# Kernel optimization log

Hardware: AMD Instinct MI355X
Metric: run time of the kernel (lower is better)

## Reference

```python
import jax, jax.numpy as jnp
import numpy as np

B, T, D, U = 8, 1024, 128, 2048
LEAK = 0.5       # leak_rate
EXPONENT = 2     # PowerIndex exponent
POW_INDEX = 2    # square neurons whose index % POW_INDEX == 0


def setup_inputs() -> dict:
    key = jax.random.key(0)
    k1, k2, k3, k4 = jax.random.split(key, 4)
    inputs = jax.random.normal(k1, (B, T, D), dtype=jnp.float32)
    # input-to-reservoir weights (InputMatrix ~ scaled dense here)
    w_in = jax.random.normal(k2, (D, U), dtype=jnp.float32) * (1.0 / np.sqrt(D))
    b_in = jax.random.uniform(k3, (U,), dtype=jnp.float32, minval=-0.05, maxval=0.05)
    # reservoir kernel (ErdosRenyi sparse random; dense surrogate scaled to
    # spectral radius ~0.9 via 0.9/sqrt(U))
    w_res = jax.random.normal(k4, (U, U), dtype=jnp.float32) * (0.9 / np.sqrt(U))
    return {"inputs": inputs, "w_in": w_in, "b_in": b_in, "w_res": w_res}


def reference(inputs, w_in, b_in, w_res):
    # Leaky ESN recurrence scanned over time:
    a = jnp.asarray(LEAK, inputs.dtype)
    # Precompute the input projection for all timesteps in one big GEMM.
    proj = jnp.einsum('btd,du->btu', inputs, w_in) + b_in  # [B,T,U]

    def step(state, p_t):  # state: [B,U], p_t: [B,U]
        pre = p_t + state @ w_res
        new = (1.0 - a) * state + a * jnp.tanh(pre)
        return new, new

    s0 = jnp.zeros((inputs.shape[0], w_res.shape[0]), inputs.dtype)
    _, states = jax.lax.scan(step, s0, jnp.swapaxes(proj, 0, 1))  # [T,B,U]
    states = jnp.swapaxes(states, 0, 1)  # [B,T,U]

    # PowerIndex: raise neurons at every POW_INDEX-th position to EXPONENT
    idx = jnp.arange(states.shape[-1])
    powered = jnp.where(idx % POW_INDEX == 0, states ** EXPONENT, states)

    # raw=False: concat input with reservoir output along features
    return jnp.concatenate([inputs, powered], axis=-1)  # [B,T,D+U]
```

## Files before the change

### kernel.cpp

```cpp
#include <hip/hip_runtime.h>
#include <cmath>

typedef __attribute__((ext_vector_type(8))) short short8;
typedef __attribute__((ext_vector_type(4))) float f32x4;
typedef __attribute__((ext_vector_type(2))) unsigned short us2;
typedef unsigned long long u64;
typedef unsigned int u32;

__device__ __forceinline__ unsigned short f2bf(float x){
  u32 u = __float_as_uint(x);
  u32 r = u + 0x7FFFu + ((u >> 16) & 1u);
  return (unsigned short)(r >> 16);
}

__global__ void bswz_kernel(const float* __restrict__ wres,
                            const float* __restrict__ win,
                            unsigned short* __restrict__ B){
  int tid = blockIdx.x * 256 + threadIdx.x;
  int l   = tid & 63;
  int cf  = tid >> 6;
  int f   = cf % 34;
  int gk  = cf / 34;
  int ks  = gk & 1;
  int gcg = gk >> 1;
  int col = (gcg << 4) + (l & 15);
  int k0  = ks * 1088 + (f << 5) + ((l >> 4) << 3);
  short8 vv;
  #pragma unroll
  for (int j = 0; j < 8; ++j){
    int k = k0 + j;
    float v = (k < 2048) ? wres[(size_t)k * 2048 + col]
                         : win[(size_t)(k - 2048) * 2048 + col];
    vv[j] = (short)f2bf(v);
  }
  *((short8*)(B + (size_t)tid * 8)) = vv;
}

__global__ void copy_in_kernel(const float* __restrict__ in, float* __restrict__ out){
  int i = blockIdx.x * 256 + threadIdx.x;
  int bt = i >> 5;
  int d4 = i & 31;
  float4 v = ((const float4*)in)[i];
  ((float4*)(out + (size_t)bt * 2176))[d4] = v;
}

__global__ void __launch_bounds__(512, 2) esn_persist(
    const float* __restrict__ inputs,
    const float* __restrict__ b_in,
    const unsigned short* __restrict__ Bsw,
    u64* __restrict__ ex,
    float* __restrict__ out)
{
  __shared__ __align__(16) unsigned short As[2 * 2176];
  __shared__ float red[2][4][16][2];

  const int tid = threadIdx.x;
  const int blk = blockIdx.x;
  const int r0  = (blk >> 5) << 1;
  const int cb  = blk & 31;
  const int wv  = tid >> 6;
  const int l   = tid & 63;
  const int m16 = l & 15;
  const int q   = l >> 4;
  const int cg  = wv >> 1;
  const int ks  = wv & 1;
  const int gcg = (cb << 2) + cg;
  const int colw0 = gcg << 4;

  short8 Bf[34];
  {
    const short8* bp = (const short8*)Bsw + (size_t)((gcg << 1) + ks) * 34 * 64 + l;
    #pragma unroll
    for (int f = 0; f < 34; ++f) Bf[f] = bp[f * 64];
  }
  const float bias = b_in[colw0 + m16];
  float s0 = 0.f, s1 = 0.f;

  const float* xr0 = inputs + (size_t)r0 * 1024 * 128;

  for (int t = 0; t < 1024; ++t){
    if (tid < 64){
      const int row = tid >> 5;
      const int seg = tid & 31;
      float4 xv = ((const float4*)(xr0 + ((size_t)row * 1024 + t) * 128))[seg];
      unsigned short* dx = &As[row * 2176 + 2048 + (seg << 2)];
      dx[0] = f2bf(xv.x); dx[1] = f2bf(xv.y); dx[2] = f2bf(xv.z); dx[3] = f2bf(xv.w);
    }
    {
      u64* srcb = ex + ((size_t)(t & 1) * 8 + r0) * 1024;
      const u32 want = (u32)t;
      u64 v[4];
      #pragma unroll
      for (int i = 0; i < 4; ++i)
        v[i] = __hip_atomic_load(&srcb[i * 512 + tid], __ATOMIC_RELAXED, __HIP_MEMORY_SCOPE_AGENT);
      u32 pend = 0xFu;
      while (pend){
        u32 np = 0;
        #pragma unroll
        for (int i = 0; i < 4; ++i)
          if (pend & (1u << i)){
            if ((u32)(v[i] >> 32) == want){
              int e = i * 512 + tid;
              us2 pr = { (unsigned short)(v[i] & 0xFFFFu), (unsigned short)((v[i] >> 16) & 0xFFFFu) };
              ((us2*)As)[(e >> 10) * 1088 + (e & 1023)] = pr;
            } else np |= (1u << i);
          }
        pend = np;
        #pragma unroll
        for (int i = 0; i < 4; ++i)
          if (pend & (1u << i))
            v[i] = __hip_atomic_load(&srcb[i * 512 + tid], __ATOMIC_RELAXED, __HIP_MEMORY_SCOPE_AGENT);
      }
    }
    __syncthreads();

    f32x4 acc0 = {0.f,0.f,0.f,0.f}, acc1 = {0.f,0.f,0.f,0.f};
    {
      const unsigned short* Ab = &As[m16 * 2176 + ks * 1088 + (q << 3)];
      const bool act = (m16 < 2);
      #pragma unroll
      for (int f = 0; f < 34; f += 2){
        short8 a0 = {0,0,0,0,0,0,0,0}, a1 = {0,0,0,0,0,0,0,0};
        if (act){
          a0 = *((const short8*)(Ab + (f << 5)));
          a1 = *((const short8*)(Ab + ((f + 1) << 5)));
        }
        acc0 = __builtin_amdgcn_mfma_f32_16x16x32_bf16(a0, Bf[f],     acc0, 0, 0, 0);
        acc1 = __builtin_amdgcn_mfma_f32_16x16x32_bf16(a1, Bf[f + 1], acc1, 0, 0, 0);
      }
    }
    float p0 = acc0[0] + acc1[0];
    float p1 = acc0[1] + acc1[1];
    if (ks == 1 && l < 16){
      red[t & 1][cg][m16][0] = p0;
      red[t & 1][cg][m16][1] = p1;
    }
    __syncthreads();

    if (ks == 0 && l < 16){
      p0 += red[t & 1][cg][m16][0];
      p1 += red[t & 1][cg][m16][1];
      float nv0 = 0.5f * s0 + 0.5f * tanhf(p0 + bias);
      float nv1 = 0.5f * s1 + 0.5f * tanhf(p1 + bias);
      s0 = nv0; s1 = nv1;
      float pv0 = __shfl_xor(nv0, 1);
      float pv1 = __shfl_xor(nv1, 1);
      const int u = colw0 + m16;
      if (!(m16 & 1)){
        u64* exw = ex + ((size_t)((t + 1) & 1) * 8 + r0) * 1024;
        u64 e0 = ((u64)(u32)(t + 1) << 32) | ((u32)f2bf(pv0) << 16) | (u32)f2bf(nv0);
        u64 e1 = ((u64)(u32)(t + 1) << 32) | ((u32)f2bf(pv1) << 16) | (u32)f2bf(nv1);
        __hip_atomic_store(&exw[u >> 1],        e0, __ATOMIC_RELAXED, __HIP_MEMORY_SCOPE_AGENT);
        __hip_atomic_store(&exw[1024 + (u >> 1)], e1, __ATOMIC_RELAXED, __HIP_MEMORY_SCOPE_AGENT);
      }
      float pw0 = (u & 1) ? nv0 : nv0 * nv0;
      float pw1 = (u & 1) ? nv1 : nv1 * nv1;
      out[((size_t)r0 * 1024 + t) * 2176 + 128 + u] = pw0;
      out[((size_t)(r0 + 1) * 1024 + t) * 2176 + 128 + u] = pw1;
    }
  }
}

extern "C" void kernel_launch(void* const* d_in, const int* in_sizes, int n_in,
                              void* d_out, int out_size, void* d_ws, size_t ws_size,
                              hipStream_t stream){
  const float* inputs = (const float*)d_in[0];
  const float* w_in   = (const float*)d_in[1];
  const float* b_in   = (const float*)d_in[2];
  const float* w_res  = (const float*)d_in[3];
  float* out = (float*)d_out;

  u64* ex = (u64*)d_ws;
  unsigned short* Bsw = (unsigned short*)((char*)d_ws + 131072);

  hipMemsetAsync(d_ws, 0, 131072, stream);
  bswz_kernel<<<2176, 256, 0, stream>>>(w_res, w_in, Bsw);
  copy_in_kernel<<<1024, 256, 0, stream>>>(inputs, out);
  esn_persist<<<128, 512, 0, stream>>>(inputs, b_in, Bsw, ex, out);
}
```

Before: 3.159 ms.

## Pack four bf16 states per exchange word with LSB parity flag

The inter-block state exchange now packs four bf16 values per 64-bit word and uses each value's least-significant mantissa bit as a phase flag instead of a 32-bit timestep tag. This halves the polled words and global stores per step. It also swaps tanhf for an exp-based fast tanh, packs the x-row conversion into one 64-bit LDS store, and removes the masked A-fragment loads by padding the LDS rows. The cost is a small precision loss from overwriting one mantissa bit, and a new init kernel is needed to seed the flag pattern.

```diff
diff --git a/kernel.cpp b/kernel.cpp
--- a/kernel.cpp
+++ b/kernel.cpp
@@ -3,14 +3,21 @@
 
 typedef __attribute__((ext_vector_type(8))) short short8;
 typedef __attribute__((ext_vector_type(4))) float f32x4;
-typedef __attribute__((ext_vector_type(2))) unsigned short us2;
 typedef unsigned long long u64;
 typedef unsigned int u32;
+
+#define RS 2208
 
 __device__ __forceinline__ unsigned short f2bf(float x){
   u32 u = __float_as_uint(x);
   u32 r = u + 0x7FFFu + ((u >> 16) & 1u);
   return (unsigned short)(r >> 16);
+}
+
+__device__ __forceinline__ float tanh_fast(float x){
+  float xc = fminf(fmaxf(x, -10.f), 10.f);
+  float e = __expf(2.f * xc);
+  return (e - 1.f) / (e + 1.f);
 }
 
 __global__ void bswz_kernel(const float* __restrict__ wres,
@@ -44,6 +51,11 @@
   ((float4*)(out + (size_t)bt * 2176))[d4] = v;
 }
 
+__global__ void exinit_kernel(u64* __restrict__ ex){
+  int i = blockIdx.x * 256 + threadIdx.x;
+  ex[i] = (i < 4096) ? 0ULL : 0x0001000100010001ULL;
+}
+
 __global__ void __launch_bounds__(512, 2) esn_persist(
     const float* __restrict__ inputs,
     const float* __restrict__ b_in,
@@ -51,7 +63,7 @@
     u64* __restrict__ ex,
     float* __restrict__ out)
 {
-  __shared__ __align__(16) unsigned short As[2 * 2176];
+  __shared__ __align__(16) unsigned short As[2 * RS];
   __shared__ float red[2][4][16][2];
 
   const int tid = threadIdx.x;
@@ -77,54 +89,47 @@
   float s0 = 0.f, s1 = 0.f;
 
   const float* xr0 = inputs + (size_t)r0 * 1024 * 128;
+  const u64 M = 0x0001000100010001ULL;
 
   for (int t = 0; t < 1024; ++t){
     if (tid < 64){
       const int row = tid >> 5;
-      const int seg = tid & 31;
-      float4 xv = ((const float4*)(xr0 + ((size_t)row * 1024 + t) * 128))[seg];
-      unsigned short* dx = &As[row * 2176 + 2048 + (seg << 2)];
-      dx[0] = f2bf(xv.x); dx[1] = f2bf(xv.y); dx[2] = f2bf(xv.z); dx[3] = f2bf(xv.w);
+      const int c   = tid & 31;
+      float4 xv = ((const float4*)(xr0 + ((size_t)row * 1024 + t) * 128))[c];
+      u64 pk = (u64)f2bf(xv.x) | ((u64)f2bf(xv.y) << 16)
+             | ((u64)f2bf(xv.z) << 32) | ((u64)f2bf(xv.w) << 48);
+      *((u64*)&As[row * RS + 2048 + (c << 2)]) = pk;
     }
     {
-      u64* srcb = ex + ((size_t)(t & 1) * 8 + r0) * 1024;
-      const u32 want = (u32)t;
-      u64 v[4];
-      #pragma unroll
-      for (int i = 0; i < 4; ++i)
-        v[i] = __hip_atomic_load(&srcb[i * 512 + tid], __ATOMIC_RELAXED, __HIP_MEMORY_SCOPE_AGENT);
-      u32 pend = 0xFu;
+      u64* srcb = ex + ((size_t)(t & 1) * 8 + r0) * 512;
+      const u64 wantm = ((t >> 1) & 1) ? M : 0ULL;
+      u64 v0 = __hip_atomic_load(&srcb[tid],       __ATOMIC_RELAXED, __HIP_MEMORY_SCOPE_AGENT);
+      u64 v1 = __hip_atomic_load(&srcb[512 + tid], __ATOMIC_RELAXED, __HIP_MEMORY_SCOPE_AGENT);
+      u32 pend = 3;
       while (pend){
         u32 np = 0;
-        #pragma unroll
-        for (int i = 0; i < 4; ++i)
-          if (pend & (1u << i)){
-            if ((u32)(v[i] >> 32) == want){
-              int e = i * 512 + tid;
-              us2 pr = { (unsigned short)(v[i] & 0xFFFFu), (unsigned short)((v[i] >> 16) & 0xFFFFu) };
-              ((us2*)As)[(e >> 10) * 1088 + (e & 1023)] = pr;
-            } else np |= (1u << i);
-          }
+        if (pend & 1){
+          if ((v0 & M) == wantm) *((u64*)&As[tid << 2]) = v0;
+          else np |= 1;
+        }
+        if (pend & 2){
+          if ((v1 & M) == wantm) *((u64*)&As[RS + (tid << 2)]) = v1;
+          else np |= 2;
+        }
         pend = np;
-        #pragma unroll
-        for (int i = 0; i < 4; ++i)
-          if (pend & (1u << i))
-            v[i] = __hip_atomic_load(&srcb[i * 512 + tid], __ATOMIC_RELAXED, __HIP_MEMORY_SCOPE_AGENT);
+        if (pend & 1) v0 = __hip_atomic_load(&srcb[tid],       __ATOMIC_RELAXED, __HIP_MEMORY_SCOPE_AGENT);
+        if (pend & 2) v1 = __hip_atomic_load(&srcb[512 + tid], __ATOMIC_RELAXED, __HIP_MEMORY_SCOPE_AGENT);
       }
     }
     __syncthreads();
 
     f32x4 acc0 = {0.f,0.f,0.f,0.f}, acc1 = {0.f,0.f,0.f,0.f};
     {
-      const unsigned short* Ab = &As[m16 * 2176 + ks * 1088 + (q << 3)];
-      const bool act = (m16 < 2);
+      const unsigned short* Ab = &As[(m16 & 1) * RS + ks * 1088 + (q << 3)];
       #pragma unroll
       for (int f = 0; f < 34; f += 2){
-        short8 a0 = {0,0,0,0,0,0,0,0}, a1 = {0,0,0,0,0,0,0,0};
-        if (act){
-          a0 = *((const short8*)(Ab + (f << 5)));
-          a1 = *((const short8*)(Ab + ((f + 1) << 5)));
-        }
+        short8 a0 = *((const short8*)(Ab + (f << 5)));
+        short8 a1 = *((const short8*)(Ab + ((f + 1) << 5)));
         acc0 = __builtin_amdgcn_mfma_f32_16x16x32_bf16(a0, Bf[f],     acc0, 0, 0, 0);
         acc1 = __builtin_amdgcn_mfma_f32_16x16x32_bf16(a1, Bf[f + 1], acc1, 0, 0, 0);
       }
@@ -140,18 +145,22 @@
     if (ks == 0 && l < 16){
       p0 += red[t & 1][cg][m16][0];
       p1 += red[t & 1][cg][m16][1];
-      float nv0 = 0.5f * s0 + 0.5f * tanhf(p0 + bias);
-      float nv1 = 0.5f * s1 + 0.5f * tanhf(p1 + bias);
+      float nv0 = 0.5f * s0 + 0.5f * tanh_fast(p0 + bias);
+      float nv1 = 0.5f * s1 + 0.5f * tanh_fast(p1 + bias);
       s0 = nv0; s1 = nv1;
-      float pv0 = __shfl_xor(nv0, 1);
-      float pv1 = __shfl_xor(nv1, 1);
+      const u32 bit = (u32)(((t + 1) >> 1) & 1);
+      u32 b0 = ((u32)f2bf(nv0) & 0xFFFEu) | bit;
+      u32 b1 = ((u32)f2bf(nv1) & 0xFFFEu) | bit;
+      u32 pr0 = b0 | (((u32)__shfl_xor((int)b0, 1)) << 16);
+      u32 pr1 = b1 | (((u32)__shfl_xor((int)b1, 1)) << 16);
+      u64 e0 = (u64)pr0 | ((u64)(u32)__shfl_xor((int)pr0, 2) << 32);
+      u64 e1 = (u64)pr1 | ((u64)(u32)__shfl_xor((int)pr1, 2) << 32);
       const int u = colw0 + m16;
-      if (!(m16 & 1)){
-        u64* exw = ex + ((size_t)((t + 1) & 1) * 8 + r0) * 1024;
-        u64 e0 = ((u64)(u32)(t + 1) << 32) | ((u32)f2bf(pv0) << 16) | (u32)f2bf(nv0);
-        u64 e1 = ((u64)(u32)(t + 1) << 32) | ((u32)f2bf(pv1) << 16) | (u32)f2bf(nv1);
-        __hip_atomic_store(&exw[u >> 1],        e0, __ATOMIC_RELAXED, __HIP_MEMORY_SCOPE_AGENT);
-        __hip_atomic_store(&exw[1024 + (u >> 1)], e1, __ATOMIC_RELAXED, __HIP_MEMORY_SCOPE_AGENT);
+      if ((m16 & 3) == 0){
+        u64* exw = ex + ((size_t)((t + 1) & 1) * 8 + r0) * 512;
+        const int p = (colw0 + m16) >> 2;
+        __hip_atomic_store(&exw[p],       e0, __ATOMIC_RELAXED, __HIP_MEMORY_SCOPE_AGENT);
+        __hip_atomic_store(&exw[512 + p], e1, __ATOMIC_RELAXED, __HIP_MEMORY_SCOPE_AGENT);
       }
       float pw0 = (u & 1) ? nv0 : nv0 * nv0;
       float pw1 = (u & 1) ? nv1 : nv1 * nv1;
@@ -171,9 +180,9 @@
   float* out = (float*)d_out;
 
   u64* ex = (u64*)d_ws;
-  unsigned short* Bsw = (unsigned short*)((char*)d_ws + 131072);
+  unsigned short* Bsw = (unsigned short*)((char*)d_ws + 65536);
 
-  hipMemsetAsync(d_ws, 0, 131072, stream);
+  exinit_kernel<<<32, 256, 0, stream>>>(ex);
   bswz_kernel<<<2176, 256, 0, stream>>>(w_res, w_in, Bsw);
   copy_in_kernel<<<1024, 256, 0, stream>>>(inputs, out);
   esn_persist<<<128, 512, 0, stream>>>(inputs, b_in, Bsw, ex, out);
```

Result: faster. 3.078 ms (-2.6%).
